# Kernel optimization log

Hardware: AMD Instinct MI355X
Metric: run time of the kernel (lower is better)

## Reference

```python
import jax, jax.numpy as jnp
from jax import lax
import numpy as np

EPS = 1e-8
NUM_ROUTES = 1152  # 32 * 6 * 6
NUM_OBJ = 10
OBJ_DIM = 16
PC_CAPS = 8
PC_CH = 32


def _squash(s, axis=-1):
    sq = jnp.sum(s * s, axis=axis, keepdims=True)
    return (sq / (1.0 + sq)) * s / jnp.sqrt(sq + EPS)


def setup_inputs() -> dict:
    key = jax.random.key(0)
    ks = jax.random.split(key, 12)
    B = 512
    image = jax.random.uniform(ks[0], (B, 1, 28, 28), dtype=jnp.float32)
    label = jax.random.randint(ks[1], (B,), 0, NUM_OBJ)
    conv_w = jax.random.normal(ks[2], (256, 1, 9, 9), dtype=jnp.float32) * 0.05
    conv_b = jnp.zeros((256,), jnp.float32)
    pc_w = jax.random.normal(ks[3], (PC_CAPS, PC_CH, 256, 9, 9), dtype=jnp.float32) * 0.02
    pc_b = jnp.zeros((PC_CAPS, PC_CH), jnp.float32)
    W_route = jax.random.normal(ks[4], (NUM_ROUTES, NUM_OBJ, OBJ_DIM, PC_CAPS), dtype=jnp.float32)
    dec_w1 = jax.random.normal(ks[5], (512, NUM_OBJ * OBJ_DIM), dtype=jnp.float32) * 0.05
    dec_b1 = jnp.zeros((512,), jnp.float32)
    dec_w2 = jax.random.normal(ks[6], (1024, 512), dtype=jnp.float32) * 0.05
    dec_b2 = jnp.zeros((1024,), jnp.float32)
    dec_w3 = jax.random.normal(ks[7], (784, 1024), dtype=jnp.float32) * 0.05
    dec_b3 = jnp.zeros((784,), jnp.float32)
    return {"image": image, "label": label, "conv_w": conv_w, "conv_b": conv_b,
            "pc_w": pc_w, "pc_b": pc_b, "W_route": W_route,
            "dec_w1": dec_w1, "dec_b1": dec_b1, "dec_w2": dec_w2, "dec_b2": dec_b2,
            "dec_w3": dec_w3, "dec_b3": dec_b3}


def reference(image, label, conv_w, conv_b, pc_w, pc_b, W_route,
              dec_w1, dec_b1, dec_w2, dec_b2, dec_w3, dec_b3):
    B = image.shape[0]
    # ConvEncoder: [B,1,28,28] -> [B,256,20,20]
    x = lax.conv_general_dilated(image, conv_w, (1, 1), 'VALID',
                                 dimension_numbers=('NCHW', 'OIHW', 'NCHW'))
    x = jax.nn.relu(x + conv_b[None, :, None, None])
    # PrimaryCaps: 8 parallel convs fused into one conv with 8*32 out channels
    pw = pc_w.reshape(PC_CAPS * PC_CH, 256, 9, 9)
    u = lax.conv_general_dilated(x, pw, (2, 2), 'VALID',
                                 dimension_numbers=('NCHW', 'OIHW', 'NCHW'))
    u = u + pc_b.reshape(-1)[None, :, None, None]  # [B,256,6,6] == stack dim=1 of [B,8,32,6,6]
    # faithful torch .view: [B,8,32,6,6] row-major -> [B,1152,8]
    u = u.reshape(B, NUM_ROUTES, PC_CAPS)
    u = _squash(u, axis=-1)
    # ObjectCaps dynamic routing
    # u_hat[b,r,j,o] = sum_c W[r,j,o,c] * u[b,r,c]
    u_hat = jnp.einsum('rjoc,brc->brjo', W_route, u)  # [B,1152,10,16]
    b_ij = jnp.zeros((B, NUM_ROUTES, NUM_OBJ), u_hat.dtype)
    v = None
    for it in range(3):
        c_ij = jax.nn.softmax(b_ij, axis=2)                  # softmax over capsules j
        s_j = jnp.einsum('brj,brjo->bjo', c_ij, u_hat)       # [B,10,16]
        v = _squash(s_j, axis=-1)
        if it < 2:
            b_ij = b_ij + jnp.einsum('brjo,bjo->brj', u_hat, v)
    obj_vectors = v[..., None]  # [B,10,16,1]
    # safe_norm over dim=2, squeeze(-1)
    y_prob = jnp.sqrt(jnp.sum(v * v, axis=-1) + EPS)  # [B,10]
    # Decoder: mask by label one-hot, MLP to reconstruction
    mask = jax.nn.one_hot(label, NUM_OBJ, dtype=v.dtype)
    masked = (v * mask[:, :, None]).reshape(B, NUM_OBJ * OBJ_DIM)
    h = jax.nn.relu(masked @ dec_w1.T + dec_b1)
    h = jax.nn.relu(h @ dec_w2.T + dec_b2)
    recon = jax.nn.sigmoid(h @ dec_w3.T + dec_b3).reshape(B, 1, 28, 28)
    return obj_vectors, recon, y_prob
```

## Files before the change

kernel.cpp:

```cpp
#include <hip/hip_runtime.h>
#include <hip/hip_bf16.h>

#define EPSF 1e-8f

typedef __attribute__((ext_vector_type(8))) short short8v;
typedef __attribute__((ext_vector_type(4))) float float4v;

static __device__ __forceinline__ unsigned short f2bf_bits(float x)
{
    return __builtin_bit_cast(unsigned short, __float2bfloat16(x));
}

__global__ __launch_bounds__(256) void k_bw2(const float* __restrict__ pw,
                                             __hip_bfloat16* __restrict__ Bw2)
{
    const int oc = blockIdx.x;
    const int t = threadIdx.x;
    __shared__ unsigned short wl[20736];
    for (int i = t; i < 20736; i += 256)
        wl[i] = f2bf_bits(pw[(size_t)oc * 20736 + i]);
    __syncthreads();
    const int r16 = oc & 15, nt = (oc >> 4) & 3, wcq = oc >> 6;
    for (int e = t; e < 2592; e += 256) {
        const int kidx = e >> 5, icc = (e >> 2) & 7, slot = e & 3;
        short8v v;
        #pragma unroll
        for (int i = 0; i < 8; ++i)
            v[i] = (short)wl[(icc * 32 + slot * 8 + i) * 81 + kidx];
        const int chunk = ((kidx * 8 + icc) * 4 + wcq) * 4 + nt;
        *(short8v*)(Bw2 + (size_t)chunk * 512 + (slot * 16 + r16) * 8) = v;
    }
}

__global__ __launch_bounds__(256) void k_conv1(const float* __restrict__ img,
                                               const float* __restrict__ cw,
                                               const float* __restrict__ cb,
                                               __hip_bfloat16* __restrict__ xt)
{
    const int b = blockIdx.x;
    const int c = threadIdx.x;
    __shared__ float simg[784];
    for (int i = c; i < 784; i += 256) simg[i] = img[b * 784 + i];
    float wreg[81];
    const float* wp = cw + c * 81;
    #pragma unroll
    for (int k = 0; k < 81; ++k) wreg[k] = wp[k];
    const float bias = cb[c];
    __syncthreads();

    const int icc = c >> 5, slot = (c >> 3) & 3, ic8 = c & 7;
    char* xbase = (char*)xt + ((size_t)b * 8 + icc) * 25600;

    for (int h = 0; h < 20; ++h) {
        for (int wg = 0; wg < 5; ++wg) {
            float acc[4] = {bias, bias, bias, bias};
            #pragma unroll
            for (int ky = 0; ky < 9; ++ky) {
                const float* rp = &simg[(h + ky) * 28 + wg * 4];
                float v[12];
                #pragma unroll
                for (int i = 0; i < 12; ++i) v[i] = rp[i];
                #pragma unroll
                for (int kx = 0; kx < 9; ++kx) {
                    const float wv = wreg[ky * 9 + kx];
                    #pragma unroll
                    for (int i = 0; i < 4; ++i)
                        acc[i] = fmaf(v[kx + i], wv, acc[i]);
                }
            }
            #pragma unroll
            for (int i = 0; i < 4; ++i) {
                int w = wg * 4 + i;
                float av = fmaxf(acc[i], 0.f);
                int pos = h * 20 + (w & 1) * 10 + (w >> 1);
                int off = pos * 64 + ((slot ^ ((pos >> 1) & 3)) << 4) + ic8 * 2;
                *(unsigned short*)(xbase + off) = f2bf_bits(av);
            }
        }
    }
}

__device__ __forceinline__ void stage_x(const __hip_bfloat16* __restrict__ xt,
                                        char* dst, int b0, int icc, int t)
{
    const __hip_bfloat16* base0 = xt + ((size_t)(b0    ) * 8 + icc) * 12800;
    const __hip_bfloat16* base1 = xt + ((size_t)(b0 + 1) * 8 + icc) * 12800;
    #pragma unroll
    for (int k = 0; k < 6; ++k) {
        const int unit = t + k * 512;
        const __hip_bfloat16* gp = (unit < 1600) ? (base0 + unit * 8)
                                                 : (base1 + (unit - 1600) * 8);
        __builtin_amdgcn_global_load_lds(
            (const __attribute__((address_space(1))) unsigned int*)gp,
            (__attribute__((address_space(3))) unsigned int*)(dst + unit * 16),
            16, 0, 0);
    }
    if (t < 128) {
        const int unit = 3072 + t;
        const __hip_bfloat16* gp = base1 + (unit - 1600) * 8;
        __builtin_amdgcn_global_load_lds(
            (const __attribute__((address_space(1))) unsigned int*)gp,
            (__attribute__((address_space(3))) unsigned int*)(dst + unit * 16),
            16, 0, 0);
    }
}

__global__ __launch_bounds__(512) void k_conv2(const __hip_bfloat16* __restrict__ xt,
                                               const __hip_bfloat16* __restrict__ Bw2,
                                               const float* __restrict__ pcb,
                                               float* __restrict__ u)
{
    const int b0 = blockIdx.x * 2;
    const int t = threadIdx.x;
    const int lane = t & 63, wid = t >> 6;
    const int wr = wid >> 2, wc = wid & 3;
    const int r16 = lane & 15, slot = lane >> 4;

    __shared__ alignas(16) char xs[2][51200];

    int lc[3];
    #pragma unroll
    for (int mt = 0; mt < 3; ++mt) {
        int hw = mt * 16 + r16;
        if (hw >= 36) hw = 0;
        int h = hw / 6, w = hw - h * 6;
        lc[mt] = 40 * h + w;
    }

    float4v acc[3][4];
    #pragma unroll
    for (int mt = 0; mt < 3; ++mt)
        #pragma unroll
        for (int nt = 0; nt < 4; ++nt)
            acc[mt][nt] = (float4v){0.f, 0.f, 0.f, 0.f};

    stage_x(xt, xs[0], b0, 0, t);
    __syncthreads();

    for (int icc = 0; icc < 8; ++icc) {
        const int cur = icc & 1;
        if (icc < 7) stage_x(xt, xs[cur ^ 1], b0, icc + 1, t);

        const char* xw = xs[cur] + wr * 25600;
        const __hip_bfloat16* bp = Bw2 + ((size_t)icc * 4 + wc) * 2048 + lane * 8;

        #pragma unroll 3
        for (int kidx = 0; kidx < 81; ++kidx) {
            int ky = kidx / 9, kx = kidx - ky * 9;
            int scalK = 20 * ky + 10 * (kx & 1) + (kx >> 1);
            short8v a[3];
            #pragma unroll
            for (int mt = 0; mt < 3; ++mt) {
                int pos = lc[mt] + scalK;
                int off = pos * 64 + (((slot ^ (pos >> 1)) & 3) << 4);
                a[mt] = *(const short8v*)(xw + off);
            }
            const __hip_bfloat16* bq = bp + (size_t)kidx * 65536;
            short8v bv[4];
            #pragma unroll
            for (int nt = 0; nt < 4; ++nt)
                bv[nt] = *(const short8v*)(bq + nt * 512);
            #pragma unroll
            for (int mt = 0; mt < 3; ++mt)
                #pragma unroll
                for (int nt = 0; nt < 4; ++nt)
                    acc[mt][nt] = __builtin_amdgcn_mfma_f32_16x16x32_bf16(a[mt], bv[nt], acc[mt][nt], 0, 0, 0);
        }
        __syncthreads();
    }

    const int b = b0 + wr;
    #pragma unroll
    for (int mt = 0; mt < 3; ++mt) {
        int hwb = mt * 16 + slot * 4;
        if (hwb < 36) {
            #pragma unroll
            for (int nt = 0; nt < 4; ++nt) {
                int oc = wc * 64 + nt * 16 + r16;
                float pb = pcb[oc];
                float4v v = acc[mt][nt];
                v.x += pb; v.y += pb; v.z += pb; v.w += pb;
                *(float4v*)(u + (size_t)b * 9216 + oc * 36 + hwb) = v;
            }
        }
    }
}

__global__ void k_squash_u(float* __restrict__ u, int ngroups)
{
    int g = blockIdx.x * blockDim.x + threadIdx.x;
    if (g >= ngroups) return;
    float4v* p = (float4v*)(u + (size_t)g * 8);
    float4v a = p[0], c = p[1];
    float sq = a.x * a.x + a.y * a.y + a.z * a.z + a.w * a.w
             + c.x * c.x + c.y * c.y + c.z * c.z + c.w * c.w;
    float scale = (sq / (1.f + sq)) / sqrtf(sq + EPSF);
    a *= scale; c *= scale;
    p[0] = a; p[1] = c;
}

__global__ __launch_bounds__(256, 2) void k_route3(const float* __restrict__ u,
                                                   const float* __restrict__ W,
                                                   const float* __restrict__ vsum,
                                                   float* __restrict__ spart, int iter)
{
    const int bid = blockIdx.x;
    const int rc = bid % 144;
    const int bc = bid / 144;
    const int r0 = rc * 8;
    const int b0 = bc * 128;
    const int t = threadIdx.x;
    const int oq = t & 3;
    const int img = t >> 2;
    const int bA = b0 + img, bB = bA + 64;

    __shared__ alignas(16) float Wl[10240];
    __shared__ alignas(16) float ul[128 * 68];

    #pragma unroll
    for (int k = 0; k < 10; ++k) {
        int e = t + k * 256;
        int rr = e / 320, rest = e - rr * 320;
        float4v val = *(const float4v*)(W + (size_t)(r0 + rr) * 1280 + rest * 4);
        int es = e ^ ((e >> 3) & 3);
        *(float4v*)(Wl + es * 4) = val;
    }
    #pragma unroll
    for (int k = 0; k < 8; ++k) {
        int e = t + k * 256;
        int im = e >> 4, f4 = e & 15;
        float4v val = *(const float4v*)(u + (size_t)(b0 + im) * 9216 + rc * 64 + f4 * 4);
        *(float4v*)(ul + im * 68 + f4 * 4) = val;
    }
    __syncthreads();

    float4v accA[10], accB[10];
    #pragma unroll
    for (int j = 0; j < 10; ++j) {
        accA[j] = (float4v){0.f, 0.f, 0.f, 0.f};
        accB[j] = (float4v){0.f, 0.f, 0.f, 0.f};
    }

    const float* upA = ul + img * 68;
    const float* upB = ul + (img + 64) * 68;

    for (int r = 0; r < 8; ++r) {
        float4v uA0 = *(const float4v*)(upA + r * 8);
        float4v uA1 = *(const float4v*)(upA + r * 8 + 4);
        float4v uB0 = *(const float4v*)(upB + r * 8);
        float4v uB1 = *(const float4v*)(upB + r * 8 + 4);
        float4v uhA[10], uhB[10];
        #pragma unroll
        for (int j = 0; j < 10; ++j) {
            #pragma unroll
            for (int oo = 0; oo < 4; ++oo) {
                int un = r * 320 + j * 32 + oq * 8 + oo * 2;
                int i0 = un ^ oq;
                int i1 = i0 ^ 1;
                float4v wlo = *(const float4v*)(Wl + i0 * 4);
                float4v whi = *(const float4v*)(Wl + i1 * 4);
                uhA[j][oo] = wlo.x * uA0.x + wlo.y * uA0.y + wlo.z * uA0.z + wlo.w * uA0.w
                           + whi.x * uA1.x + whi.y * uA1.y + whi.z * uA1.z + whi.w * uA1.w;
                uhB[j][oo] = wlo.x * uB0.x + wlo.y * uB0.y + wlo.z * uB0.z + wlo.w * uB0.w
                           + whi.x * uB1.x + whi.y * uB1.y + whi.z * uB1.z + whi.w * uB1.w;
            }
        }
        if (iter > 0) {
            #pragma unroll 2
            for (int half = 0; half < 2; ++half) {
                const int b = half ? bB : bA;
                float4v* uh = half ? uhB : uhA;
                float4v* acc = half ? accB : accA;
                float q[10];
                #pragma unroll
                for (int j = 0; j < 10; ++j) {
                    float4v vj = *(const float4v*)(vsum + (size_t)b * 160 + j * 16 + oq * 4);
                    float qp = uh[j].x * vj.x + uh[j].y * vj.y
                             + uh[j].z * vj.z + uh[j].w * vj.w;
                    qp += __shfl_xor(qp, 1);
                    qp += __shfl_xor(qp, 2);
                    q[j] = qp;
                }
                float mx = q[0];
                #pragma unroll
                for (int j = 1; j < 10; ++j) mx = fmaxf(mx, q[j]);
                float ssum = 0.f;
                float c[10];
                #pragma unroll
                for (int j = 0; j < 10; ++j) { c[j] = __expf(q[j] - mx); ssum += c[j]; }
                float inv = 1.f / ssum;
                #pragma unroll
                for (int j = 0; j < 10; ++j) acc[j] += (c[j] * inv) * uh[j];
            }
        } else {
            #pragma unroll
            for (int j = 0; j < 10; ++j) {
                accA[j] += 0.1f * uhA[j];
                accB[j] += 0.1f * uhB[j];
            }
        }
    }

    float* dstA = spart + ((size_t)rc * 512 + bA) * 160 + oq * 4;
    float* dstB = spart + ((size_t)rc * 512 + bB) * 160 + oq * 4;
    #pragma unroll
    for (int j = 0; j < 10; ++j) {
        *(float4v*)(dstA + j * 16) = accA[j];
        *(float4v*)(dstB + j * 16) = accB[j];
    }
}

__global__ void k_finish(const float* __restrict__ spart, float* __restrict__ vsum,
                         const int* __restrict__ label, float* __restrict__ obj,
                         float* __restrict__ yprob, float* __restrict__ masked, int iter)
{
    const int b = blockIdx.x, t = threadIdx.x;
    if (t < 160) {
        const float* sp = spart + (size_t)b * 160 + t;
        float sv = 0.f;
        #pragma unroll 8
        for (int rc = 0; rc < 144; ++rc)
            sv += sp[(size_t)rc * 81920];
        float sq = sv * sv;
        sq += __shfl_xor(sq, 1); sq += __shfl_xor(sq, 2);
        sq += __shfl_xor(sq, 4); sq += __shfl_xor(sq, 8);
        float v = sv * (sq / (1.f + sq)) / sqrtf(sq + EPSF);
        float pv = (iter > 0) ? vsum[b * 160 + t] : 0.f;
        vsum[b * 160 + t] = pv + v;
        if (iter == 2) {
            obj[b * 160 + t] = v;
            float vv = v * v;
            vv += __shfl_xor(vv, 1); vv += __shfl_xor(vv, 2);
            vv += __shfl_xor(vv, 4); vv += __shfl_xor(vv, 8);
            int j = t >> 4;
            if ((t & 15) == 0) yprob[b * 10 + j] = sqrtf(vv + EPSF);
            masked[b * 160 + t] = (label[b] == j) ? v : 0.f;
        }
    }
}

__global__ void k_mlp(const float* __restrict__ A, const float* __restrict__ Wt,
                      const float* __restrict__ bias, float* __restrict__ C,
                      int N, int K, int act)
{
    const int m0 = blockIdx.x * 32;
    const int n0 = blockIdx.y * 32;
    const int t  = threadIdx.x;
    const int tn = t & 31, tg = t >> 5;
    __shared__ float As[32][33];
    __shared__ float Ws[32][33];
    float acc[4] = {0.f, 0.f, 0.f, 0.f};
    for (int k0 = 0; k0 < K; k0 += 32) {
        __syncthreads();
        for (int idx = t; idx < 1024; idx += 256) {
            int rr = idx >> 5, kk = idx & 31;
            As[rr][kk] = A[(size_t)(m0 + rr) * K + k0 + kk];
            int n = n0 + rr;
            Ws[rr][kk] = (n < N) ? Wt[(size_t)n * K + k0 + kk] : 0.f;
        }
        __syncthreads();
        #pragma unroll 8
        for (int kk = 0; kk < 32; ++kk) {
            float bv = Ws[tn][kk];
            #pragma unroll
            for (int i = 0; i < 4; ++i)
                acc[i] += As[tg * 4 + i][kk] * bv;
        }
    }
    int n = n0 + tn;
    if (n < N) {
        float bs = bias[n];
        #pragma unroll
        for (int i = 0; i < 4; ++i) {
            float vv = acc[i] + bs;
            vv = (act == 0) ? fmaxf(vv, 0.f) : 1.f / (1.f + expf(-vv));
            C[(size_t)(m0 + tg * 4 + i) * N + n] = vv;
        }
    }
}

extern "C" void kernel_launch(void* const* d_in, const int* in_sizes, int n_in,
                              void* d_out, int out_size, void* d_ws, size_t ws_size,
                              hipStream_t stream)
{
    const float* image  = (const float*)d_in[0];
    const int*   label  = (const int*)  d_in[1];
    const float* conv_w = (const float*)d_in[2];
    const float* conv_b = (const float*)d_in[3];
    const float* pc_w   = (const float*)d_in[4];
    const float* pc_b   = (const float*)d_in[5];
    const float* Wrt    = (const float*)d_in[6];
    const float* dw1 = (const float*)d_in[7];
    const float* db1 = (const float*)d_in[8];
    const float* dw2 = (const float*)d_in[9];
    const float* db2 = (const float*)d_in[10];
    const float* dw3 = (const float*)d_in[11];
    const float* db3 = (const float*)d_in[12];
    float* out = (float*)d_out;

    char* p = (char*)d_ws;
    __hip_bfloat16* xt  = (__hip_bfloat16*)p; p += 104857600;
    float* u      = (float*)p; p += 18874368;
    __hip_bfloat16* Bw2 = (__hip_bfloat16*)p; p += 10616832;
    float* vsum   = (float*)p; p += 327680;
    float* masked = (float*)p; p += 327680;
    float* h1     = (float*)p; p += 1048576;
    float* h2     = (float*)p; p += 2097152;

    float* spart = (float*)xt;

    float* obj   = out;
    float* recon = out + 81920;
    float* yprob = out + 483328;

    k_bw2<<<256, 256, 0, stream>>>(pc_w, Bw2);
    k_conv1<<<512, 256, 0, stream>>>(image, conv_w, conv_b, xt);
    k_conv2<<<256, 512, 0, stream>>>(xt, Bw2, pc_b, u);
    k_squash_u<<<2304, 256, 0, stream>>>(u, 589824);
    for (int it = 0; it < 3; ++it) {
        k_route3<<<576, 256, 0, stream>>>(u, Wrt, vsum, spart, it);
        k_finish<<<512, 192, 0, stream>>>(spart, vsum, label, obj, yprob, masked, it);
    }
    k_mlp<<<dim3(16, 16), 256, 0, stream>>>(masked, dw1, db1, h1, 512, 160, 0);
    k_mlp<<<dim3(16, 32), 256, 0, stream>>>(h1, dw2, db2, h2, 1024, 512, 0);
    k_mlp<<<dim3(16, 25), 256, 0, stream>>>(h2, dw3, db3, recon, 784, 1024, 1);
}
```

Baseline: 764.0 us.

## Merge two images into one 80-row M tile per wave and drop LDS double buffering

The conv2 kernel goes from 512 to 256 threads. Each wave now covers both images' 72 output rows, packed as 5 M-tiles of 16, instead of each of two wave rows doing 3 tiles for one image. Each B-fragment load from global memory therefore feeds 20 MFMAs instead of 12, which halves redundant weight loads per block. In exchange the LDS double buffer is replaced by a single buffer with syncs around staging, so loads no longer overlap compute, and the extra accumulators raise register pressure (launch bounds ask for 3 blocks).

```diff
diff --git a/kernel.cpp b/kernel.cpp
--- a/kernel.cpp
+++ b/kernel.cpp
@@ -86,8 +86,8 @@
     const __hip_bfloat16* base0 = xt + ((size_t)(b0    ) * 8 + icc) * 12800;
     const __hip_bfloat16* base1 = xt + ((size_t)(b0 + 1) * 8 + icc) * 12800;
     #pragma unroll
-    for (int k = 0; k < 6; ++k) {
-        const int unit = t + k * 512;
+    for (int k = 0; k < 12; ++k) {
+        const int unit = t + k * 256;
         const __hip_bfloat16* gp = (unit < 1600) ? (base0 + unit * 8)
                                                  : (base1 + (unit - 1600) * 8);
         __builtin_amdgcn_global_load_lds(
@@ -105,55 +105,53 @@
     }
 }
 
-__global__ __launch_bounds__(512) void k_conv2(const __hip_bfloat16* __restrict__ xt,
-                                               const __hip_bfloat16* __restrict__ Bw2,
-                                               const float* __restrict__ pcb,
-                                               float* __restrict__ u)
+__global__ __launch_bounds__(256, 3) void k_conv2(const __hip_bfloat16* __restrict__ xt,
+                                                  const __hip_bfloat16* __restrict__ Bw2,
+                                                  const float* __restrict__ pcb,
+                                                  float* __restrict__ u)
 {
     const int b0 = blockIdx.x * 2;
     const int t = threadIdx.x;
-    const int lane = t & 63, wid = t >> 6;
-    const int wr = wid >> 2, wc = wid & 3;
+    const int lane = t & 63, wc = t >> 6;
     const int r16 = lane & 15, slot = lane >> 4;
 
-    __shared__ alignas(16) char xs[2][51200];
-
-    int lc[3];
-    #pragma unroll
-    for (int mt = 0; mt < 3; ++mt) {
-        int hw = mt * 16 + r16;
-        if (hw >= 36) hw = 0;
+    __shared__ alignas(16) char xs[51200];
+
+    int aimg[5], lc[5];
+    #pragma unroll
+    for (int mt = 0; mt < 5; ++mt) {
+        int grow = mt * 16 + r16;
+        int img = (grow >= 36 && grow < 72) ? 1 : 0;
+        int hw = (grow < 72) ? (grow - 36 * img) : 0;
         int h = hw / 6, w = hw - h * 6;
+        aimg[mt] = img * 25600;
         lc[mt] = 40 * h + w;
     }
 
-    float4v acc[3][4];
-    #pragma unroll
-    for (int mt = 0; mt < 3; ++mt)
+    float4v acc[5][4];
+    #pragma unroll
+    for (int mt = 0; mt < 5; ++mt)
         #pragma unroll
         for (int nt = 0; nt < 4; ++nt)
             acc[mt][nt] = (float4v){0.f, 0.f, 0.f, 0.f};
 
-    stage_x(xt, xs[0], b0, 0, t);
-    __syncthreads();
-
     for (int icc = 0; icc < 8; ++icc) {
-        const int cur = icc & 1;
-        if (icc < 7) stage_x(xt, xs[cur ^ 1], b0, icc + 1, t);
-
-        const char* xw = xs[cur] + wr * 25600;
+        __syncthreads();
+        stage_x(xt, xs, b0, icc, t);
+        __syncthreads();
+
         const __hip_bfloat16* bp = Bw2 + ((size_t)icc * 4 + wc) * 2048 + lane * 8;
 
         #pragma unroll 3
         for (int kidx = 0; kidx < 81; ++kidx) {
             int ky = kidx / 9, kx = kidx - ky * 9;
             int scalK = 20 * ky + 10 * (kx & 1) + (kx >> 1);
-            short8v a[3];
-            #pragma unroll
-            for (int mt = 0; mt < 3; ++mt) {
+            short8v a[5];
+            #pragma unroll
+            for (int mt = 0; mt < 5; ++mt) {
                 int pos = lc[mt] + scalK;
-                int off = pos * 64 + (((slot ^ (pos >> 1)) & 3) << 4);
-                a[mt] = *(const short8v*)(xw + off);
+                int off = aimg[mt] + pos * 64 + (((slot ^ (pos >> 1)) & 3) << 4);
+                a[mt] = *(const short8v*)(xs + off);
             }
             const __hip_bfloat16* bq = bp + (size_t)kidx * 65536;
             short8v bv[4];
@@ -161,19 +159,20 @@
             for (int nt = 0; nt < 4; ++nt)
                 bv[nt] = *(const short8v*)(bq + nt * 512);
             #pragma unroll
-            for (int mt = 0; mt < 3; ++mt)
+            for (int mt = 0; mt < 5; ++mt)
                 #pragma unroll
                 for (int nt = 0; nt < 4; ++nt)
                     acc[mt][nt] = __builtin_amdgcn_mfma_f32_16x16x32_bf16(a[mt], bv[nt], acc[mt][nt], 0, 0, 0);
         }
-        __syncthreads();
-    }
-
-    const int b = b0 + wr;
-    #pragma unroll
-    for (int mt = 0; mt < 3; ++mt) {
-        int hwb = mt * 16 + slot * 4;
-        if (hwb < 36) {
+    }
+
+    #pragma unroll
+    for (int mt = 0; mt < 5; ++mt) {
+        int grow0 = mt * 16 + slot * 4;
+        if (grow0 < 72) {
+            int img = grow0 >= 36;
+            int hwb = grow0 - 36 * img;
+            const int b = b0 + img;
             #pragma unroll
             for (int nt = 0; nt < 4; ++nt) {
                 int oc = wc * 64 + nt * 16 + r16;
@@ -415,7 +414,7 @@
 
     k_bw2<<<256, 256, 0, stream>>>(pc_w, Bw2);
     k_conv1<<<512, 256, 0, stream>>>(image, conv_w, conv_b, xt);
-    k_conv2<<<256, 512, 0, stream>>>(xt, Bw2, pc_b, u);
+    k_conv2<<<256, 256, 0, stream>>>(xt, Bw2, pc_b, u);
     k_squash_u<<<2304, 256, 0, stream>>>(u, 589824);
     for (int it = 0; it < 3; ++it) {
         k_route3<<<576, 256, 0, stream>>>(u, Wrt, vsum, spart, it);
```

New measurement: 872.2 us. 1.14x slower.
